# Performance work log

Hardware: AMD Instinct MI355X
Metric: run time of the kernel (lower is better)

## Reference

```python
import jax, jax.numpy as jnp
import numpy as np

N = 100000      # nodes
E = 3200000     # edges (avg degree 32)
IN, HID, OUT = 512, 256, 64
K = 10
ALPHA = 0.1


def setup_inputs() -> dict:
    key = jax.random.key(0)
    k1, k2, k3, k4 = jax.random.split(key, 4)
    x = jax.random.normal(k1, (N, IN), dtype=jnp.float32)
    edge_index = jax.random.randint(k2, (2, E), 0, N, dtype=jnp.int64)
    # MLP params (Kaiming-ish scaling)
    W1 = jax.random.normal(k3, (IN, HID), dtype=jnp.float32) / np.sqrt(IN)
    b1 = jnp.zeros((HID,), dtype=jnp.float32)
    W2 = jax.random.normal(k4, (HID, OUT), dtype=jnp.float32) / np.sqrt(HID)
    b2 = jnp.zeros((OUT,), dtype=jnp.float32)
    # GPR_prop PPR init: temp[k] = alpha*(1-alpha)^k, temp[K] = (1-alpha)^K
    ks = np.arange(K + 1)
    temp = ALPHA * (1.0 - ALPHA) ** ks
    temp[-1] = (1.0 - ALPHA) ** K
    temp = jnp.asarray(temp, dtype=jnp.float32)
    return {"x": x, "edge_index": edge_index, "W1": W1, "b1": b1,
            "W2": W2, "b2": b2, "temp": temp}


def reference(x, edge_index, W1, b1, W2, b2, temp):
    # MLP front-end (eval mode: dropout = identity)
    h = jax.nn.relu(x @ W1 + b1)
    h = h @ W2 + b2                                  # [N, OUT]

    # gcn_norm with self-loops: A_hat = D^{-1/2} (A + I) D^{-1/2}
    loop = jnp.arange(N, dtype=edge_index.dtype)
    src = jnp.concatenate([edge_index[0], loop])      # [E+N]
    dst = jnp.concatenate([edge_index[1], loop])      # [E+N]
    deg = jax.ops.segment_sum(jnp.ones_like(dst, dtype=h.dtype), dst,
                              num_segments=N)
    dis = jnp.where(deg > 0, jax.lax.rsqrt(deg), 0.0)
    norm = (dis[src] * dis[dst])[:, None]             # [E+N, 1]

    # GPR propagation: out = sum_k temp[k] * A_hat^k h
    def step(carry, gamma):
        hk, acc = carry
        hk = jax.ops.segment_sum(norm * hk[src], dst, num_segments=N)
        return (hk, acc + gamma * hk), None

    (_, out), _ = jax.lax.scan(step, (h, temp[0] * h), temp[1:])
    return out
```

## Files before the change

### kernel.cpp

```cpp
#include <hip/hip_runtime.h>

#define NN 100000
#define NE 3200000
#define DIN 512
#define DHID 256
#define DOUT 64
#define KPROP 10

typedef _Float16 f16;
typedef _Float16 f16x8 __attribute__((ext_vector_type(8)));
typedef _Float16 f16x4 __attribute__((ext_vector_type(4)));
typedef float f32x4 __attribute__((ext_vector_type(4)));

__global__ void detect_i64(const int* __restrict__ ei, int* __restrict__ flag) {
  int lane = threadIdx.x;
  int ok = 1;
  for (int i = lane; i < 512; i += 64)
    if (ei[2 * i + 1] != 0) ok = 0;
  ok = __all(ok);
  if (lane == 0) *flag = ok;
}

__global__ void zero_cnt(int* __restrict__ cnt) {
  int g = blockIdx.x * blockDim.x + threadIdx.x;
  if (g < NN) cnt[g] = 0;
}

__global__ void count_deg(const int* __restrict__ ei, const int* __restrict__ flag,
                          int* __restrict__ cnt) {
  int g = blockIdx.x * blockDim.x + threadIdx.x;
  int e0 = g * 4;
  if (e0 >= NE) return;
  int is64 = *flag;
  int d0, d1, d2, d3;
  if (is64) {
    int4 a = *(const int4*)&ei[2 * (size_t)NE + 2 * (size_t)e0];
    int4 b = *(const int4*)&ei[2 * (size_t)NE + 2 * (size_t)e0 + 4];
    d0 = a.x; d1 = a.z; d2 = b.x; d3 = b.z;
  } else {
    int4 a = *(const int4*)&ei[(size_t)NE + e0];
    d0 = a.x; d1 = a.y; d2 = a.z; d3 = a.w;
  }
  atomicAdd(&cnt[d0], 1);
  atomicAdd(&cnt[d1], 1);
  atomicAdd(&cnt[d2], 1);
  atomicAdd(&cnt[d3], 1);
}

__global__ void scan1(const int* __restrict__ cnt, int* __restrict__ rs,
                      int* __restrict__ bsum) {
  __shared__ int tmp[1024];
  int t = threadIdx.x;
  int g = blockIdx.x * 1024 + t;
  int v = (g < NN) ? cnt[g] : 0;
  tmp[t] = v;
  __syncthreads();
  for (int off = 1; off < 1024; off <<= 1) {
    int y = (t >= off) ? tmp[t - off] : 0;
    __syncthreads();
    tmp[t] += y;
    __syncthreads();
  }
  if (g < NN) rs[g] = tmp[t] - v;
  if (t == 1023) bsum[blockIdx.x] = tmp[t];
}

__global__ void scan2(int* __restrict__ bsum, int nb) {
  if (blockIdx.x == 0 && threadIdx.x == 0) {
    int s = 0;
    for (int i = 0; i < nb; i++) { int v = bsum[i]; bsum[i] = s; s += v; }
  }
}

__global__ void scan3_and_dis(int* __restrict__ rs, const int* __restrict__ bsum,
                              int* __restrict__ cursor, const int* __restrict__ cnt,
                              float* __restrict__ dis) {
  int g = blockIdx.x * blockDim.x + threadIdx.x;
  if (g < NN) {
    int v = rs[g] + bsum[g >> 10];
    rs[g] = v;
    cursor[g] = v;
    dis[g] = rsqrtf((float)(cnt[g] + 1));
  }
}

__global__ void fill_csr(const int* __restrict__ ei, const int* __restrict__ flag,
                         const float* __restrict__ dis, int* __restrict__ cursor,
                         int2* __restrict__ recs) {
  int g = blockIdx.x * blockDim.x + threadIdx.x;
  int e0 = g * 2;
  if (e0 >= NE) return;
  int is64 = *flag;
  int s0, s1, d0, d1;
  if (is64) {
    int4 sv = *(const int4*)&ei[2 * (size_t)e0];
    int4 dv = *(const int4*)&ei[2 * (size_t)NE + 2 * (size_t)e0];
    s0 = sv.x; s1 = sv.z; d0 = dv.x; d1 = dv.z;
  } else {
    int2 sv = *(const int2*)&ei[e0];
    int2 dv = *(const int2*)&ei[(size_t)NE + e0];
    s0 = sv.x; s1 = sv.y; d0 = dv.x; d1 = dv.y;
  }
  int p0 = atomicAdd(&cursor[d0], 1);
  recs[p0] = make_int2(s0, __float_as_int(dis[s0] * dis[d0]));
  int p1 = atomicAdd(&cursor[d1], 1);
  recs[p1] = make_int2(s1, __float_as_int(dis[s1] * dis[d1]));
}

__global__ void cvt_weights(const float* __restrict__ W1, const float* __restrict__ W2,
                            f16* __restrict__ W1t, f16* __restrict__ W2t) {
  int g = blockIdx.x * 256 + threadIdx.x;
  if (g < DIN * DHID) {
    int k = g >> 8, n = g & 255;
    W1t[(size_t)n * DIN + k] = (f16)W1[g];
  }
  if (g < DHID * DOUT) {
    int k = g >> 6, n = g & 63;
    W2t[(size_t)n * DHID + k] = (f16)W2[g];
  }
}

__global__ __launch_bounds__(256) void mlp_mfma(
    const float* __restrict__ x, const f16* __restrict__ W1t,
    const float* __restrict__ b1, const f16* __restrict__ W2t,
    const float* __restrict__ b2, const float* __restrict__ temp,
    f16* __restrict__ h, f16* __restrict__ z)
{
  __shared__ __align__(16) char smraw[2 * 64 * 136 * 2];
  f16* xsb = (f16*)smraw;
  f16* h1s = (f16*)smraw;
  int t = threadIdx.x;
  int lane = t & 63;
  int w = t >> 6;
  int n0 = blockIdx.x * 64;
  int r15 = lane & 15;
  int g4 = lane >> 4;
  int nbase = w * 64;
  int srow = t >> 5, sc4 = t & 31;

  f32x4 acc[4][4];
  #pragma unroll
  for (int nt = 0; nt < 4; nt++) {
    float bv = b1[nbase + nt * 16 + r15];
    #pragma unroll
    for (int mt = 0; mt < 4; mt++) acc[mt][nt] = (f32x4){bv, bv, bv, bv};
  }

  float4 ld[8];
  #pragma unroll
  for (int it = 0; it < 8; it++) {
    int row = srow + it * 8;
    int gr = n0 + row;
    ld[it] = (gr < NN) ? *(const float4*)&x[(size_t)gr * DIN + sc4 * 4]
                       : make_float4(0.f, 0.f, 0.f, 0.f);
  }
  #pragma unroll
  for (int it = 0; it < 8; it++) {
    int row = srow + it * 8;
    f16x4 hv = { (f16)ld[it].x, (f16)ld[it].y, (f16)ld[it].z, (f16)ld[it].w };
    *(f16x4*)&xsb[row * 136 + sc4 * 4] = hv;
  }
  __syncthreads();

  for (int c = 0; c < 4; c++) {
    int cur = c & 1;
    if (c < 3) {
      #pragma unroll
      for (int it = 0; it < 8; it++) {
        int row = srow + it * 8;
        int gr = n0 + row;
        ld[it] = (gr < NN)
            ? *(const float4*)&x[(size_t)gr * DIN + (c + 1) * 128 + sc4 * 4]
            : make_float4(0.f, 0.f, 0.f, 0.f);
      }
    }
    int k0 = c * 128;
    const f16* xs = xsb + cur * 8704;
    #pragma unroll
    for (int ks = 0; ks < 4; ks++) {
      int kk = ks * 32 + g4 * 8;
      f16x8 a[4], b[4];
      #pragma unroll
      for (int mt = 0; mt < 4; mt++)
        a[mt] = *(const f16x8*)&xs[(mt * 16 + r15) * 136 + kk];
      #pragma unroll
      for (int nt = 0; nt < 4; nt++)
        b[nt] = *(const f16x8*)&W1t[(size_t)(nbase + nt * 16 + r15) * DIN + k0 + kk];
      #pragma unroll
      for (int mt = 0; mt < 4; mt++)
        #pragma unroll
        for (int nt = 0; nt < 4; nt++)
          acc[mt][nt] = __builtin_amdgcn_mfma_f32_16x16x32_f16(a[mt], b[nt], acc[mt][nt], 0, 0, 0);
    }
    if (c < 3) {
      #pragma unroll
      for (int it = 0; it < 8; it++) {
        int row = srow + it * 8;
        f16x4 hv = { (f16)ld[it].x, (f16)ld[it].y, (f16)ld[it].z, (f16)ld[it].w };
        *(f16x4*)&xsb[(cur ^ 1) * 8704 + row * 136 + sc4 * 4] = hv;
      }
    }
    __syncthreads();
  }

  #pragma unroll
  for (int mt = 0; mt < 4; mt++)
    #pragma unroll
    for (int nt = 0; nt < 4; nt++)
      #pragma unroll
      for (int r = 0; r < 4; r++) {
        float v = fmaxf(acc[mt][nt][r], 0.f);
        h1s[(mt * 16 + g4 * 4 + r) * 264 + nbase + nt * 16 + r15] = (f16)v;
      }
  __syncthreads();

  f32x4 acc2[4];
  #pragma unroll
  for (int nt = 0; nt < 4; nt++) {
    float bv = b2[nt * 16 + r15];
    acc2[nt] = (f32x4){bv, bv, bv, bv};
  }
  #pragma unroll
  for (int ks = 0; ks < 8; ks++) {
    int kk = ks * 32 + g4 * 8;
    f16x8 a2 = *(const f16x8*)&h1s[(w * 16 + r15) * 264 + kk];
    #pragma unroll
    for (int nt = 0; nt < 4; nt++) {
      f16x8 bf = *(const f16x8*)&W2t[(size_t)(nt * 16 + r15) * DHID + kk];
      acc2[nt] = __builtin_amdgcn_mfma_f32_16x16x32_f16(a2, bf, acc2[nt], 0, 0, 0);
    }
  }
  float tK = temp[KPROP];
  #pragma unroll
  for (int nt = 0; nt < 4; nt++)
    #pragma unroll
    for (int r = 0; r < 4; r++) {
      int node = n0 + w * 16 + g4 * 4 + r;
      if (node < NN) {
        int colv = nt * 16 + r15;
        float v = acc2[nt][r];
        h[(size_t)node * DOUT + colv] = (f16)v;
        z[(size_t)node * DOUT + colv] = (f16)(tK * v);
      }
    }
}

__global__ __launch_bounds__(256) void prop_horner(
    const f16* __restrict__ z, f16* __restrict__ zn, const f16* __restrict__ h,
    float* __restrict__ out, const int* __restrict__ rs, const int* __restrict__ cnt,
    const int2* __restrict__ recs, const float* __restrict__ dis,
    const float* __restrict__ temp, int kidx, int final_step)
{
  int w = blockIdx.x * 4 + (threadIdx.x >> 6);
  int lane = threadIdx.x & 63;
  if (w >= NN) return;
  int q = lane >> 3;
  int s8 = lane & 7;

  float acc[8];
  #pragma unroll
  for (int f = 0; f < 8; f++) acc[f] = 0.f;

  int beg = rs[w], n = cnt[w];
  const int2* rp = recs + beg;

  int e = 0;
  for (; e + 32 <= n; e += 32) {
    int2 r0 = rp[e + q];
    int2 r1 = rp[e + 8 + q];
    int2 r2 = rp[e + 16 + q];
    int2 r3 = rp[e + 24 + q];
    f16x8 g0 = *(const f16x8*)&z[(size_t)r0.x * DOUT + s8 * 8];
    f16x8 g1 = *(const f16x8*)&z[(size_t)r1.x * DOUT + s8 * 8];
    f16x8 g2 = *(const f16x8*)&z[(size_t)r2.x * DOUT + s8 * 8];
    f16x8 g3 = *(const f16x8*)&z[(size_t)r3.x * DOUT + s8 * 8];
    float w0 = __int_as_float(r0.y);
    float w1 = __int_as_float(r1.y);
    float w2 = __int_as_float(r2.y);
    float w3 = __int_as_float(r3.y);
    #pragma unroll
    for (int f = 0; f < 8; f++) acc[f] = fmaf(w0, (float)g0[f], acc[f]);
    #pragma unroll
    for (int f = 0; f < 8; f++) acc[f] = fmaf(w1, (float)g1[f], acc[f]);
    #pragma unroll
    for (int f = 0; f < 8; f++) acc[f] = fmaf(w2, (float)g2[f], acc[f]);
    #pragma unroll
    for (int f = 0; f < 8; f++) acc[f] = fmaf(w3, (float)g3[f], acc[f]);
  }
  for (; e + 8 <= n; e += 8) {
    int2 r0 = rp[e + q];
    f16x8 g0 = *(const f16x8*)&z[(size_t)r0.x * DOUT + s8 * 8];
    float w0 = __int_as_float(r0.y);
    #pragma unroll
    for (int f = 0; f < 8; f++) acc[f] = fmaf(w0, (float)g0[f], acc[f]);
  }
  if (e < n) {
    int rem = n - e;
    int qq = q < rem ? q : rem - 1;
    int2 r0 = rp[e + qq];
    f16x8 g0 = *(const f16x8*)&z[(size_t)r0.x * DOUT + s8 * 8];
    float w0 = (q < rem) ? __int_as_float(r0.y) : 0.f;
    #pragma unroll
    for (int f = 0; f < 8; f++) acc[f] = fmaf(w0, (float)g0[f], acc[f]);
  }

  #pragma unroll
  for (int f = 0; f < 8; f++) {
    acc[f] += __shfl_xor(acc[f], 8);
    acc[f] += __shfl_xor(acc[f], 16);
    acc[f] += __shfl_xor(acc[f], 32);
  }

  if (q == 0) {
    float dd = dis[w];
    float dd2 = dd * dd;
    float gk = temp[kidx];
    f16x8 zs = *(const f16x8*)&z[(size_t)w * DOUT + s8 * 8];
    f16x8 hs = *(const f16x8*)&h[(size_t)w * DOUT + s8 * 8];
    #pragma unroll
    for (int f = 0; f < 8; f++)
      acc[f] += dd2 * (float)zs[f] + gk * (float)hs[f];
    if (final_step) {
      float4 o0 = { acc[0], acc[1], acc[2], acc[3] };
      float4 o1 = { acc[4], acc[5], acc[6], acc[7] };
      *(float4*)&out[(size_t)w * DOUT + s8 * 8] = o0;
      *(float4*)&out[(size_t)w * DOUT + s8 * 8 + 4] = o1;
    } else {
      f16x8 o;
      #pragma unroll
      for (int f = 0; f < 8; f++) o[f] = (f16)acc[f];
      *(f16x8*)&zn[(size_t)w * DOUT + s8 * 8] = o;
    }
  }
}

extern "C" void kernel_launch(void* const* d_in, const int* in_sizes, int n_in,
                              void* d_out, int out_size, void* d_ws, size_t ws_size,
                              hipStream_t stream) {
  const float* x    = (const float*)d_in[0];
  const int*   ei   = (const int*)d_in[1];
  const float* W1   = (const float*)d_in[2];
  const float* b1   = (const float*)d_in[3];
  const float* W2   = (const float*)d_in[4];
  const float* b2   = (const float*)d_in[5];
  const float* temp = (const float*)d_in[6];
  float* out = (float*)d_out;

  char* wsb = (char*)d_ws;
  size_t off = 0;
  auto carve = [&](size_t bytes) -> void* {
    void* p = wsb + off;
    off = (off + bytes + 255) & ~(size_t)255;
    return p;
  };
  int*   cnt    = (int*)carve((size_t)NN * 4);
  int*   rs     = (int*)carve((size_t)NN * 4);
  int*   cursor = (int*)carve((size_t)NN * 4);
  int*   bsum   = (int*)carve(128 * 4);
  int*   flag   = (int*)carve(256);
  float* dis    = (float*)carve((size_t)NN * 4);
  int2*  recs   = (int2*)carve((size_t)NE * 8);
  f16*   W1t    = (f16*)carve((size_t)DHID * DIN * 2);
  f16*   W2t    = (f16*)carve((size_t)DOUT * DHID * 2);
  f16*   h_buf  = (f16*)carve((size_t)NN * DOUT * 2);
  f16*   z_a    = (f16*)carve((size_t)NN * DOUT * 2);
  f16*   z_b    = (f16*)carve((size_t)NN * DOUT * 2);
  if (off > ws_size) return;

  detect_i64<<<1, 64, 0, stream>>>(ei, flag);
  zero_cnt<<<(NN + 255) / 256, 256, 0, stream>>>(cnt);
  count_deg<<<(NE / 4 + 255) / 256, 256, 0, stream>>>(ei, flag, cnt);
  scan1<<<(NN + 1023) / 1024, 1024, 0, stream>>>(cnt, rs, bsum);
  scan2<<<1, 64, 0, stream>>>(bsum, (NN + 1023) / 1024);
  scan3_and_dis<<<(NN + 255) / 256, 256, 0, stream>>>(rs, bsum, cursor, cnt, dis);
  fill_csr<<<(NE / 2 + 255) / 256, 256, 0, stream>>>(ei, flag, dis, cursor, recs);

  cvt_weights<<<(DIN * DHID + 255) / 256, 256, 0, stream>>>(W1, W2, W1t, W2t);
  mlp_mfma<<<(NN + 63) / 64, 256, 0, stream>>>(x, W1t, b1, W2t, b2, temp, h_buf, z_a);

  const f16* zc = z_a;
  f16* zn = z_b;
  for (int k = KPROP - 1; k >= 0; k--) {
    prop_horner<<<(NN + 3) / 4, 256, 0, stream>>>(zc, zn, h_buf, out, rs, cnt,
                                                  recs, dis, temp, k, k == 0);
    const f16* t2 = zn;
    zn = (f16*)zc;
    zc = t2;
  }
}
```

Measured before the change: 1.031 ms.

## Partition degree count and CSR fill by destination range across blocks

The degree-count and CSR-fill kernels now launch eight times as many blocks. Each block handles a 1024-edge chunk but only performs atomics for destinations inside one of eight node ranges. Block index interleaves partitions so that concurrently running blocks aim their atomics at distinct, smaller address ranges, with the goal of better L2 locality for the atomics and scattered record writes. In exchange, the edge-index array is read eight times over, and the fill kernel issues per-edge scalar source loads.

```diff
diff --git a/kernel.cpp b/kernel.cpp
--- a/kernel.cpp
+++ b/kernel.cpp
@@ -6,6 +6,8 @@
 #define DHID 256
 #define DOUT 64
 #define KPROP 10
+#define NPART 8
+#define PSZ 12500
 
 typedef _Float16 f16;
 typedef _Float16 f16x8 __attribute__((ext_vector_type(8)));
@@ -26,10 +28,12 @@
   if (g < NN) cnt[g] = 0;
 }
 
-__global__ void count_deg(const int* __restrict__ ei, const int* __restrict__ flag,
-                          int* __restrict__ cnt) {
-  int g = blockIdx.x * blockDim.x + threadIdx.x;
-  int e0 = g * 4;
+__global__ __launch_bounds__(256) void count_deg(
+    const int* __restrict__ ei, const int* __restrict__ flag,
+    int* __restrict__ cnt) {
+  int p = blockIdx.x & 7;
+  int chunk = blockIdx.x >> 3;
+  int e0 = chunk * 1024 + threadIdx.x * 4;
   if (e0 >= NE) return;
   int is64 = *flag;
   int d0, d1, d2, d3;
@@ -41,10 +45,11 @@
     int4 a = *(const int4*)&ei[(size_t)NE + e0];
     d0 = a.x; d1 = a.y; d2 = a.z; d3 = a.w;
   }
-  atomicAdd(&cnt[d0], 1);
-  atomicAdd(&cnt[d1], 1);
-  atomicAdd(&cnt[d2], 1);
-  atomicAdd(&cnt[d3], 1);
+  int lo = p * PSZ, hi = lo + PSZ;
+  if (d0 >= lo && d0 < hi) atomicAdd(&cnt[d0], 1);
+  if (d1 >= lo && d1 < hi) atomicAdd(&cnt[d1], 1);
+  if (d2 >= lo && d2 < hi) atomicAdd(&cnt[d2], 1);
+  if (d3 >= lo && d3 < hi) atomicAdd(&cnt[d3], 1);
 }
 
 __global__ void scan1(const int* __restrict__ cnt, int* __restrict__ rs,
@@ -84,27 +89,33 @@
   }
 }
 
-__global__ void fill_csr(const int* __restrict__ ei, const int* __restrict__ flag,
-                         const float* __restrict__ dis, int* __restrict__ cursor,
-                         int2* __restrict__ recs) {
-  int g = blockIdx.x * blockDim.x + threadIdx.x;
-  int e0 = g * 2;
+__global__ __launch_bounds__(256) void fill_csr(
+    const int* __restrict__ ei, const int* __restrict__ flag,
+    const float* __restrict__ dis, int* __restrict__ cursor,
+    int2* __restrict__ recs) {
+  int p = blockIdx.x & 7;
+  int chunk = blockIdx.x >> 3;
+  int e0 = chunk * 1024 + threadIdx.x * 4;
   if (e0 >= NE) return;
   int is64 = *flag;
-  int s0, s1, d0, d1;
+  int d[4];
   if (is64) {
-    int4 sv = *(const int4*)&ei[2 * (size_t)e0];
-    int4 dv = *(const int4*)&ei[2 * (size_t)NE + 2 * (size_t)e0];
-    s0 = sv.x; s1 = sv.z; d0 = dv.x; d1 = dv.z;
+    int4 a = *(const int4*)&ei[2 * (size_t)NE + 2 * (size_t)e0];
+    int4 b = *(const int4*)&ei[2 * (size_t)NE + 2 * (size_t)e0 + 4];
+    d[0] = a.x; d[1] = a.z; d[2] = b.x; d[3] = b.z;
   } else {
-    int2 sv = *(const int2*)&ei[e0];
-    int2 dv = *(const int2*)&ei[(size_t)NE + e0];
-    s0 = sv.x; s1 = sv.y; d0 = dv.x; d1 = dv.y;
-  }
-  int p0 = atomicAdd(&cursor[d0], 1);
-  recs[p0] = make_int2(s0, __float_as_int(dis[s0] * dis[d0]));
-  int p1 = atomicAdd(&cursor[d1], 1);
-  recs[p1] = make_int2(s1, __float_as_int(dis[s1] * dis[d1]));
+    int4 a = *(const int4*)&ei[(size_t)NE + e0];
+    d[0] = a.x; d[1] = a.y; d[2] = a.z; d[3] = a.w;
+  }
+  int lo = p * PSZ, hi = lo + PSZ;
+  #pragma unroll
+  for (int j = 0; j < 4; j++) {
+    if (d[j] >= lo && d[j] < hi) {
+      int s = is64 ? ei[2 * (size_t)(e0 + j)] : ei[e0 + j];
+      int pos = atomicAdd(&cursor[d[j]], 1);
+      recs[pos] = make_int2(s, __float_as_int(dis[s] * dis[d[j]]));
+    }
+  }
 }
 
 __global__ void cvt_weights(const float* __restrict__ W1, const float* __restrict__ W2,
@@ -367,13 +378,15 @@
   f16*   z_b    = (f16*)carve((size_t)NN * DOUT * 2);
   if (off > ws_size) return;
 
+  int nchunks = NE / 1024;
+
   detect_i64<<<1, 64, 0, stream>>>(ei, flag);
   zero_cnt<<<(NN + 255) / 256, 256, 0, stream>>>(cnt);
-  count_deg<<<(NE / 4 + 255) / 256, 256, 0, stream>>>(ei, flag, cnt);
+  count_deg<<<nchunks * NPART, 256, 0, stream>>>(ei, flag, cnt);
   scan1<<<(NN + 1023) / 1024, 1024, 0, stream>>>(cnt, rs, bsum);
   scan2<<<1, 64, 0, stream>>>(bsum, (NN + 1023) / 1024);
   scan3_and_dis<<<(NN + 255) / 256, 256, 0, stream>>>(rs, bsum, cursor, cnt, dis);
-  fill_csr<<<(NE / 2 + 255) / 256, 256, 0, stream>>>(ei, flag, dis, cursor, recs);
+  fill_csr<<<nchunks * NPART, 256, 0, stream>>>(ei, flag, dis, cursor, recs);
 
   cvt_weights<<<(DIN * DHID + 255) / 256, 256, 0, stream>>>(W1, W2, W1t, W2t);
   mlp_mfma<<<(NN + 63) / 64, 256, 0, stream>>>(x, W1t, b1, W2t, b2, temp, h_buf, z_a);
```

Result: no change. 1.017 ms (-1.3%).
